# Kernel optimization log

Measured on AMD Instinct MI355X. Metric: run time of the kernel, lower is better.

Reference implementation:

```python
import jax, jax.numpy as jnp
import numpy as np

B, H, W, L, C = 4, 64, 64, 64, 64
NB, BS, F = 8, 8, 1          # num_blocks, block_size, hidden_size_factor
R, ALPHA = 8, 1.0            # lora_r, lora_alpha
M, T = 32, 8                 # modes, temporal_modes
SCALE = 1.0 / (BS * BS * F)  # param init scale from the module


def setup_inputs() -> dict:
    key = jax.random.key(0)
    ks = jax.random.split(key, 14)
    d = {"x": jax.random.normal(ks[0], (B, H, W, L, C), jnp.float32)}
    d["w1"] = SCALE * jax.random.uniform(ks[1], (2, NB, BS, BS * F), jnp.float32)
    d["b1"] = SCALE * jax.random.uniform(ks[2], (2, NB, BS * F), jnp.float32)
    d["w2"] = SCALE * jax.random.uniform(ks[3], (2, NB, BS * F, BS), jnp.float32)
    d["b2"] = SCALE * jax.random.uniform(ks[4], (2, NB, BS), jnp.float32)
    names = ["la1rA", "la1rB", "la1iA", "la1iB", "la2rA", "la2rB", "la2iA", "la2iB"]
    shapes = [(NB, BS, R), (NB, R, BS * F), (NB, BS, R), (NB, R, BS * F),
              (NB, BS * F, R), (NB, R, BS), (NB, BS * F, R), (NB, R, BS)]
    for i, (n, s) in enumerate(zip(names, shapes)):
        d[n] = 0.02 * jax.random.normal(ks[5 + i], s, jnp.float32)
    return d


def _afno(x, w1, b1, w2, b2, la1rA, la1rB, la1iA, la1iB, la2rA, la2rB, la2iA, la2iB):
    s = ALPHA / R
    # effective per-block weights: base + LoRA low-rank update  [NB, in, out]
    W1r = w1[0] + s * jnp.einsum('nir,nro->nio', la1rA, la1rB)
    W1i = w1[1] + s * jnp.einsum('nir,nro->nio', la1iA, la1iB)
    W2r = w2[0] + s * jnp.einsum('nir,nro->nio', la2rA, la2rB)
    W2i = w2[1] + s * jnp.einsum('nir,nro->nio', la2iA, la2iB)

    xf = jnp.fft.rfftn(x, axes=(1, 2, 3), norm='ortho')      # [B,H,W,L//2+1,C] complex
    Lh = xf.shape[3]
    xs = xf[:, :M, :M, :T].reshape(B, M, M, T, NB, BS)        # truncated modes, block split
    xr, xi = xs.real, xs.imag

    def lin(v, Wb, bb):  # block-diagonal linear: [...,n,i] x [n,i,o] + [n,o]
        return jnp.einsum('bxyzni,nio->bxyzno', v, Wb) + bb

    gelu = lambda t: jax.nn.gelu(t, approximate=False)
    o1r = gelu(lin(xr, W1r, b1[0]) - lin(xi, W1i, b1[1]))
    o1i = gelu(lin(xi, W1r, b1[0]) + lin(xr, W1i, b1[1]))
    o2r = lin(o1r, W2r, b2[0]) - lin(o1i, W2i, b2[1])
    o2i = lin(o1i, W2r, b2[0]) + lin(o1r, W2i, b2[1])

    o2 = (o2r + 1j * o2i).reshape(B, M, M, T, C)
    full = jnp.zeros((B, H, W, Lh, C), dtype=xf.dtype).at[:, :M, :M, :T].set(o2)
    out = jnp.fft.irfftn(full, s=(H, W, L), axes=(1, 2, 3), norm='ortho')
    return out + x


def reference(x, w1, b1, w2, b2, la1rA, la1rB, la1iA, la1iB, la2rA, la2rB, la2iA, la2iB):
    return _afno(x, w1, b1, w2, b2, la1rA, la1rB, la1iA, la1iB, la2rA, la2rB, la2iA, la2iB)
```

## Files before the change

### kernel.cpp

```cpp
#include <hip/hip_runtime.h>
#include <math.h>


#define PI2_64 0.09817477042468103f

__device__ __forceinline__ float gelu_exact(float t) {
    return 0.5f * t * (1.0f + erff(t * 0.7071067811865475f));
}

__global__ void __launch_bounds__(256) k1a_dft_l(const float* __restrict__ x,
                                                 float* __restrict__ y1f) {
    __shared__ float2 twT[8][32];
    int tid = threadIdx.x;
    if (tid < 256) {
        int k = tid >> 5, l = tid & 31;
        float s, c;
        sincosf(PI2_64 * (float)((k * l) & 63), &s, &c);
        twT[k][l] = make_float2(c, s);
    }
    __syncthreads();

    int bid = blockIdx.x;
    int w8 = bid & 7, bh = bid >> 3;
    int cp = tid & 31, wl = tid >> 5;
    int w = w8 * 8 + wl;
    const float* xp = x + (size_t)(bh * 64 + w) * 4096 + 2 * cp;

    float4 A[8];
#pragma unroll
    for (int kl = 0; kl < 8; ++kl) A[kl] = make_float4(0.f, 0.f, 0.f, 0.f);

    for (int l0 = 0; l0 < 32; l0 += 2) {
        float2 v0  = *(const float2*)(xp + (l0 + 0) * 64);
        float2 v0p = *(const float2*)(xp + (l0 + 32) * 64);
        float2 v1  = *(const float2*)(xp + (l0 + 1) * 64);
        float2 v1p = *(const float2*)(xp + (l0 + 33) * 64);
        float2 E0 = make_float2(v0.x + v0p.x, v0.y + v0p.y);
        float2 O0 = make_float2(v0.x - v0p.x, v0.y - v0p.y);
        float2 E1 = make_float2(v1.x + v1p.x, v1.y + v1p.y);
        float2 O1 = make_float2(v1.x - v1p.x, v1.y - v1p.y);
#pragma unroll
        for (int kl = 0; kl < 8; ++kl) {
            float2 t0 = twT[kl][l0];
            float2 t1 = twT[kl][l0 + 1];
            float2 s0 = (kl & 1) ? O0 : E0;
            float2 s1 = (kl & 1) ? O1 : E1;
            A[kl].x += s0.x * t0.x;  A[kl].y -= s0.x * t0.y;
            A[kl].z += s0.y * t0.x;  A[kl].w -= s0.y * t0.y;
            A[kl].x += s1.x * t1.x;  A[kl].y -= s1.x * t1.y;
            A[kl].z += s1.y * t1.x;  A[kl].w -= s1.y * t1.y;
        }
    }
    float4* y1 = (float4*)y1f;
    size_t base = (size_t)bh * 16384 + (size_t)w * 32 + cp;
#pragma unroll
    for (int kl = 0; kl < 8; ++kl)
        y1[base + kl * 2048] = A[kl];
}

__global__ void __launch_bounds__(256) k1b_dft_w(const float* __restrict__ y1f,
                                                 float* __restrict__ y2f) {
    __shared__ float4 sD[64 * 32];
    __shared__ float2 twT[32][32];
    int tid = threadIdx.x;
#pragma unroll
    for (int e = 0; e < 4; ++e) {
        int idx = e * 256 + tid;
        int k = idx >> 5, l = idx & 31;
        float s, c;
        sincosf(PI2_64 * (float)((k * l) & 63), &s, &c);
        twT[k][l] = make_float2(c, s);
    }
    int pos = blockIdx.x;
    int kl = pos & 7, bh = pos >> 3;
    const float4* src = (const float4*)y1f + (size_t)pos * 2048;
#pragma unroll
    for (int r = 0; r < 8; ++r)
        sD[r * 256 + tid] = src[r * 256 + tid];
    __syncthreads();

    int cp = tid & 31, kwg = tid >> 5;
    float4 acc[4];
#pragma unroll
    for (int i = 0; i < 4; ++i) acc[i] = make_float4(0.f, 0.f, 0.f, 0.f);

    for (int w = 0; w < 32; ++w) {
        float4 d  = sD[w * 32 + cp];
        float4 dp = sD[(w + 32) * 32 + cp];
        float4 E = make_float4(d.x + dp.x, d.y + dp.y, d.z + dp.z, d.w + dp.w);
        float4 O = make_float4(d.x - dp.x, d.y - dp.y, d.z - dp.z, d.w - dp.w);
#pragma unroll
        for (int i = 0; i < 4; ++i) {
            float2 t = twT[kwg * 4 + i][w];
            float4 s = (i & 1) ? O : E;
            acc[i].x += s.x * t.x + s.y * t.y;
            acc[i].y += s.y * t.x - s.x * t.y;
            acc[i].z += s.z * t.x + s.w * t.y;
            acc[i].w += s.w * t.x - s.z * t.y;
        }
    }
    int b = bh >> 6, h = bh & 63;
    float4* y2 = (float4*)y2f;
#pragma unroll
    for (int i = 0; i < 4; ++i) {
        int kw = kwg * 4 + i;
        y2[((size_t)((b * 8 + kl) * 32 + kw) * 64 + h) * 32 + cp] = acc[i];
    }
}

__global__ void __launch_bounds__(256) kc_h_mlp(
        const float* __restrict__ y2f, float* __restrict__ z2f,
        const float* __restrict__ w1, const float* __restrict__ b1,
        const float* __restrict__ w2, const float* __restrict__ b2,
        const float* __restrict__ la1rA, const float* __restrict__ la1rB,
        const float* __restrict__ la1iA, const float* __restrict__ la1iB,
        const float* __restrict__ la2rA, const float* __restrict__ la2rB,
        const float* __restrict__ la2iA, const float* __restrict__ la2iB) {
    __shared__ float2 sD[64][64];
    __shared__ float2 sT[32][34];
    __shared__ float2 sM[32][66];
    __shared__ float  sW[4][512];
    __shared__ float  sb1[128], sb2[128];
    int tid = threadIdx.x;
    int pos = blockIdx.x;
    int kl = pos & 7, kw = (pos >> 3) & 31, b = pos >> 8;

#pragma unroll
    for (int r = 0; r < 4; ++r) {
        int idx = r * 256 + tid;
        int h = idx >> 5, kh = idx & 31;
        float sn, cs;
        sincosf(PI2_64 * (float)((h * kh) & 63), &sn, &cs);
        sT[h][kh] = make_float2(cs, -sn);
    }
    const float2* src = (const float2*)y2f + (size_t)((b * 8 + kl) * 32 + kw) * 4096;
#pragma unroll
    for (int r = 0; r < 8; ++r) {
        int f = r * 512 + tid * 2;
        *(float4*)(&sD[f >> 6][f & 63]) = *(const float4*)(src + f);
    }
    {
        const float* As[4]   = {la1rA, la1iA, la2rA, la2iA};
        const float* Bs[4]   = {la1rB, la1iB, la2rB, la2iB};
        const float* base[4] = {w1, w1 + 512, w2, w2 + 512};
#pragma unroll
        for (int e = 0; e < 8; ++e) {
            int flat = tid + e * 256;
            int mat = flat >> 9;
            int rem = flat & 511;
            int n = rem >> 6, i = (rem >> 3) & 7, o = rem & 7;
            const float* A  = As[mat] + n * 64 + i * 8;
            const float* Bp = Bs[mat] + n * 64 + o;
            float s = 0.f;
#pragma unroll
            for (int r = 0; r < 8; ++r) s += A[r] * Bp[r * 8];
            sW[mat][(i * 8 + o) * 8 + n] = base[mat][n * 64 + i * 8 + o] + 0.125f * s;
        }
        if (tid < 128) sb1[tid] = b1[tid];
        else           sb2[tid - 128] = b2[tid - 128];
    }
    __syncthreads();

    {
        float4* sd4 = (float4*)&sD[0][0];
#pragma unroll
        for (int r = 0; r < 4; ++r) {
            int idx = r * 256 + tid;
            int h = idx >> 5, cq = idx & 31;
            float4 a = sd4[h * 32 + cq];
            float4 c = sd4[(h + 32) * 32 + cq];
            sd4[h * 32 + cq]        = make_float4(a.x + c.x, a.y + c.y, a.z + c.z, a.w + c.w);
            sd4[(h + 32) * 32 + cq] = make_float4(a.x - c.x, a.y - c.y, a.z - c.z, a.w - c.w);
        }
    }
    __syncthreads();

    {
        int kh0 = (tid >> 5) * 4;
        int c0  = (tid & 31) * 2;
        float mr[4][2], mi[4][2];
#pragma unroll
        for (int i = 0; i < 4; ++i)
#pragma unroll
            for (int j = 0; j < 2; ++j) { mr[i][j] = 0.f; mi[i][j] = 0.f; }
        for (int h = 0; h < 32; ++h) {
            float4 dE = *(const float4*)(&sD[h][c0]);
            float4 dO = *(const float4*)(&sD[h + 32][c0]);
            float Er[2] = {dE.x, dE.z}, Ei[2] = {dE.y, dE.w};
            float Or[2] = {dO.x, dO.z}, Oi[2] = {dO.y, dO.w};
            const float4* tT = (const float4*)(&sT[h][kh0]);
            float4 u0 = tT[0], u1 = tT[1];
            float Tr[4] = {u0.x, u0.z, u1.x, u1.z};
            float Ti[4] = {u0.y, u0.w, u1.y, u1.w};
#pragma unroll
            for (int i = 0; i < 4; ++i) {
                const float* Dr = (i & 1) ? Or : Er;
                const float* Di = (i & 1) ? Oi : Ei;
#pragma unroll
                for (int j = 0; j < 2; ++j) {
                    mr[i][j] += Tr[i] * Dr[j] - Ti[i] * Di[j];
                    mi[i][j] += Tr[i] * Di[j] + Ti[i] * Dr[j];
                }
            }
        }
        const float sc = 1.0f / 512.0f;
#pragma unroll
        for (int i = 0; i < 4; ++i)
#pragma unroll
            for (int j = 0; j < 2; ++j)
                sM[kh0 + i][c0 + j] = make_float2(mr[i][j] * sc, mi[i][j] * sc);
    }
    __syncthreads();

    float2* sM2 = (float2*)&sD[0][0];
    {
        int kh = tid >> 3, n = tid & 7;
        float xr[8], xi[8];
#pragma unroll
        for (int i = 0; i < 8; ++i) {
            float2 v = sM[kh][n * 8 + i];
            xr[i] = v.x; xi[i] = v.y;
        }
        float o1r[8], o1i[8];
#pragma unroll
        for (int o = 0; o < 8; ++o) {
            float br = sb1[n * 8 + o], bi = sb1[64 + n * 8 + o];
            float sr = br - bi, si = br + bi;
#pragma unroll
            for (int i = 0; i < 8; ++i) {
                float wr = sW[0][(i * 8 + o) * 8 + n];
                float wi = sW[1][(i * 8 + o) * 8 + n];
                sr += xr[i] * wr - xi[i] * wi;
                si += xi[i] * wr + xr[i] * wi;
            }
            o1r[o] = gelu_exact(sr);
            o1i[o] = gelu_exact(si);
        }
#pragma unroll
        for (int o = 0; o < 8; ++o) {
            float br = sb2[n * 8 + o], bi = sb2[64 + n * 8 + o];
            float sr = br - bi, si = br + bi;
#pragma unroll
            for (int i = 0; i < 8; ++i) {
                float wr = sW[2][(i * 8 + o) * 8 + n];
                float wi = sW[3][(i * 8 + o) * 8 + n];
                sr += o1r[i] * wr - o1i[i] * wi;
                si += o1i[i] * wr + o1r[i] * wi;
            }
            sM2[kh * 66 + n * 8 + o] = make_float2(sr, si);
        }
    }
    __syncthreads();

    {
        int h0 = (tid >> 4) * 2;
        int c0 = (tid & 15) * 4;
        float SEr[2][4], SEi[2][4], SOr[2][4], SOi[2][4];
#pragma unroll
        for (int r = 0; r < 2; ++r)
#pragma unroll
            for (int j = 0; j < 4; ++j) {
                SEr[r][j] = 0.f; SEi[r][j] = 0.f;
                SOr[r][j] = 0.f; SOi[r][j] = 0.f;
            }
        for (int khp = 0; khp < 16; ++khp) {
#pragma unroll
            for (int par = 0; par < 2; ++par) {
                int kh = 2 * khp + par;
                float2 T0 = sT[h0 + 0][kh];
                float2 T1 = sT[h0 + 1][kh];
                const float4* tM = (const float4*)(sM2 + kh * 66 + c0);
                float4 m0 = tM[0], m1 = tM[1];
                float Mr[4] = {m0.x, m0.z, m1.x, m1.z};
                float Mi[4] = {m0.y, m0.w, m1.y, m1.w};
                float (*Sr)[4] = par ? SOr : SEr;
                float (*Si)[4] = par ? SOi : SEi;
                float Tr[2] = {T0.x, T1.x};
                float Ti[2] = {T0.y, T1.y};
#pragma unroll
                for (int r = 0; r < 2; ++r)
#pragma unroll
                    for (int j = 0; j < 4; ++j) {
                        Sr[r][j] += Tr[r] * Mr[j] + Ti[r] * Mi[j];
                        Si[r][j] += Tr[r] * Mi[j] - Ti[r] * Mr[j];
                    }
            }
        }
        float2* dst = (float2*)z2f + (size_t)((b * 8 + kl) * 32 + kw) * 4096;
#pragma unroll
        for (int r = 0; r < 2; ++r) {
            float4* dA = (float4*)(dst + (h0 + r) * 64 + c0);
            dA[0] = make_float4(SEr[r][0] + SOr[r][0], SEi[r][0] + SOi[r][0],
                                SEr[r][1] + SOr[r][1], SEi[r][1] + SOi[r][1]);
            dA[1] = make_float4(SEr[r][2] + SOr[r][2], SEi[r][2] + SOi[r][2],
                                SEr[r][3] + SOr[r][3], SEi[r][3] + SOi[r][3]);
            float4* dB = (float4*)(dst + (h0 + 32 + r) * 64 + c0);
            dB[0] = make_float4(SEr[r][0] - SOr[r][0], SEi[r][0] - SOi[r][0],
                                SEr[r][1] - SOr[r][1], SEi[r][1] - SOi[r][1]);
            dB[1] = make_float4(SEr[r][2] - SOr[r][2], SEi[r][2] - SOi[r][2],
                                SEr[r][3] - SOr[r][3], SEi[r][3] - SOi[r][3]);
        }
    }
}

__global__ void __launch_bounds__(256) k3a_idft_w(const float* __restrict__ z2f,
                                                  float* __restrict__ zwf) {
    __shared__ float4 sZ[2 * 32 * 32];
    __shared__ float2 twT[32][32];
    int tid = threadIdx.x;
#pragma unroll
    for (int e = 0; e < 4; ++e) {
        int idx = e * 256 + tid;
        int w = idx >> 5, kw = idx & 31;
        float s, c;
        sincosf(PI2_64 * (float)((w * kw) & 63), &s, &c);
        twT[w][kw] = make_float2(c, s);
    }
    int bid = blockIdx.x;
    int klq = bid & 3, h = (bid >> 2) & 63, b = bid >> 8;
    const float4* z2 = (const float4*)z2f;
#pragma unroll
    for (int r = 0; r < 8; ++r) {
        int idx = r * 256 + tid;
        int row = idx >> 5, cp2 = idx & 31;
        int kli = row >> 5, kw = row & 31;
        sZ[idx] = z2[((size_t)((b * 8 + klq * 2 + kli) * 32 + kw) * 64 + h) * 32 + cp2];
    }
    __syncthreads();

    int cp = tid & 31, wq = tid >> 5;

    float4 E[2][4], O[2][4];
#pragma unroll
    for (int kli = 0; kli < 2; ++kli)
#pragma unroll
        for (int j = 0; j < 4; ++j) {
            E[kli][j] = make_float4(0.f, 0.f, 0.f, 0.f);
            O[kli][j] = make_float4(0.f, 0.f, 0.f, 0.f);
        }

    for (int kw = 0; kw < 32; kw += 2) {
#pragma unroll
        for (int kli = 0; kli < 2; ++kli) {
            float4 d = sZ[(kli * 32 + kw) * 32 + cp];
#pragma unroll
            for (int j = 0; j < 4; ++j) {
                float2 t = twT[wq * 4 + j][kw];
                E[kli][j].x += d.x * t.x - d.y * t.y;
                E[kli][j].y += d.y * t.x + d.x * t.y;
                E[kli][j].z += d.z * t.x - d.w * t.y;
                E[kli][j].w += d.w * t.x + d.z * t.y;
            }
        }
#pragma unroll
        for (int kli = 0; kli < 2; ++kli) {
            float4 d = sZ[(kli * 32 + kw + 1) * 32 + cp];
#pragma unroll
            for (int j = 0; j < 4; ++j) {
                float2 t = twT[wq * 4 + j][kw + 1];
                O[kli][j].x += d.x * t.x - d.y * t.y;
                O[kli][j].y += d.y * t.x + d.x * t.y;
                O[kli][j].z += d.z * t.x - d.w * t.y;
                O[kli][j].w += d.w * t.x + d.z * t.y;
            }
        }
    }
    float4* zw = (float4*)zwf;
    size_t slab = ((size_t)(b * 64 + h)) * 16384;
#pragma unroll
    for (int kli = 0; kli < 2; ++kli) {
        int kl = klq * 2 + kli;
#pragma unroll
        for (int j = 0; j < 4; ++j) {
            int w = wq * 4 + j;
            float4 e = E[kli][j], o = O[kli][j];
            zw[slab + ((size_t)w * 8 + kl) * 32 + cp] =
                make_float4(e.x + o.x, e.y + o.y, e.z + o.z, e.w + o.w);
            zw[slab + ((size_t)(w + 32) * 8 + kl) * 32 + cp] =
                make_float4(e.x - o.x, e.y - o.y, e.z - o.z, e.w - o.w);
        }
    }
}

__global__ void __launch_bounds__(256) k3b_idft_l(const float* __restrict__ x,
                                                  const float* __restrict__ zwf,
                                                  float* __restrict__ outp) {
    __shared__ float2 twA[8][32];
    int tid = threadIdx.x;
    if (tid < 256) {
        int k = tid >> 5, l = tid & 31;
        float s, c;
        sincosf(PI2_64 * (float)((k * l) & 63), &s, &c);
        twA[k][l] = make_float2(c, s);
    }
    __syncthreads();

    int bid = blockIdx.x;
    int w8 = bid & 7, bh = bid >> 3;
    int cp = tid & 31, wl = tid >> 5;
    int w = w8 * 8 + wl;

    const float4* zw = (const float4*)zwf +
        ((size_t)bh * 64 + w) * 256 + cp;
    float4 z[8];
#pragma unroll
    for (int kl = 0; kl < 8; ++kl) z[kl] = zw[kl * 32];

    float z0r0 = z[0].x, z0r1 = z[0].z;
#pragma unroll
    for (int kl = 1; kl < 8; ++kl) {
        z[kl].x *= 2.f; z[kl].y *= 2.f; z[kl].z *= 2.f; z[kl].w *= 2.f;
    }
    const size_t row = ((size_t)(bh * 64 + w)) * 4096;
    const float* xp = x + row + 2 * cp;
    float* op = outp + row + 2 * cp;
    const float sc = 1.0f / 512.0f;

    for (int l = 0; l < 32; ++l) {
        float2 a0 = *(const float2*)(xp + l * 64);
        float2 a1 = *(const float2*)(xp + (l + 32) * 64);
        float e0 = 0.f, e1 = 0.f, o0 = 0.f, o1 = 0.f;
#pragma unroll
        for (int kl = 2; kl < 8; kl += 2) {
            float2 t = twA[kl][l];
            e0 += z[kl].x * t.x - z[kl].y * t.y;
            e1 += z[kl].z * t.x - z[kl].w * t.y;
        }
#pragma unroll
        for (int kl = 1; kl < 8; kl += 2) {
            float2 t = twA[kl][l];
            o0 += z[kl].x * t.x - z[kl].y * t.y;
            o1 += z[kl].z * t.x - z[kl].w * t.y;
        }
        float base0 = z0r0 + e0, base1 = z0r1 + e1;
        *(float2*)(op + l * 64) =
            make_float2((base0 + o0) * sc + a0.x, (base1 + o1) * sc + a0.y);
        *(float2*)(op + (l + 32) * 64) =
            make_float2((base0 - o0) * sc + a1.x, (base1 - o1) * sc + a1.y);
    }
}

extern "C" void kernel_launch(void* const* d_in, const int* in_sizes, int n_in,
                              void* d_out, int out_size, void* d_ws, size_t ws_size,
                              hipStream_t stream) {
    const float* x     = (const float*)d_in[0];
    const float* w1    = (const float*)d_in[1];
    const float* b1    = (const float*)d_in[2];
    const float* w2    = (const float*)d_in[3];
    const float* b2    = (const float*)d_in[4];
    const float* la1rA = (const float*)d_in[5];
    const float* la1rB = (const float*)d_in[6];
    const float* la1iA = (const float*)d_in[7];
    const float* la1iB = (const float*)d_in[8];
    const float* la2rA = (const float*)d_in[9];
    const float* la2rB = (const float*)d_in[10];
    const float* la2iA = (const float*)d_in[11];
    const float* la2iB = (const float*)d_in[12];
    float* out = (float*)d_out;

    float* ws = (float*)d_ws;
    float* y1 = ws;
    float* y2 = ws + 16777216;
    float* z2 = ws + 25165824;
    float* zw = ws + 33554432;

    hipLaunchKernelGGL(k1a_dft_l,  dim3(2048), dim3(256), 0, stream, x, y1);
    hipLaunchKernelGGL(k1b_dft_w,  dim3(2048), dim3(256), 0, stream, y1, y2);
    hipLaunchKernelGGL(kc_h_mlp,   dim3(1024), dim3(256), 0, stream, y2, z2,
                       w1, b1, w2, b2, la1rA, la1rB, la1iA, la1iB,
                       la2rA, la2rB, la2iA, la2iB);
    hipLaunchKernelGGL(k3a_idft_w, dim3(1024), dim3(256), 0, stream, z2, zw);
    hipLaunchKernelGGL(k3b_idft_l, dim3(2048), dim3(256), 0, stream, x, zw, out);
}
```

Measured before the change: 320.5 us.

## Store all inter-kernel spectral intermediates as bf16 to halve workspace traffic

Every intermediate buffer passed between the five DFT/MLP kernels (y1, y2, z2, zw) is now packed to bfloat16 with round-to-nearest-even and unpacked to fp32 on load. All arithmetic stays in fp32. The goal is to halve the global memory bytes written and read between stages, which dominate this memory-bound pipeline. The cost is reduced precision in the spectral intermediates, which adds error to the output and could break a tight tolerance.

```diff
diff --git a/kernel.cpp b/kernel.cpp
--- a/kernel.cpp
+++ b/kernel.cpp
@@ -8,8 +8,23 @@
     return 0.5f * t * (1.0f + erff(t * 0.7071067811865475f));
 }
 
+__device__ __forceinline__ unsigned int f2bf(float f) {
+    unsigned int u = __float_as_uint(f);
+    return (u + 0x7FFFu + ((u >> 16) & 1u)) >> 16;
+}
+__device__ __forceinline__ uint2 pack4(float4 f) {
+    return make_uint2(f2bf(f.x) | (f2bf(f.y) << 16),
+                      f2bf(f.z) | (f2bf(f.w) << 16));
+}
+__device__ __forceinline__ float4 unpack4(uint2 u) {
+    return make_float4(__uint_as_float(u.x << 16),
+                       __uint_as_float(u.x & 0xFFFF0000u),
+                       __uint_as_float(u.y << 16),
+                       __uint_as_float(u.y & 0xFFFF0000u));
+}
+
 __global__ void __launch_bounds__(256) k1a_dft_l(const float* __restrict__ x,
-                                                 float* __restrict__ y1f) {
+                                                 unsigned int* __restrict__ y1f) {
     __shared__ float2 twT[8][32];
     int tid = threadIdx.x;
     if (tid < 256) {
@@ -51,15 +66,15 @@
             A[kl].z += s1.y * t1.x;  A[kl].w -= s1.y * t1.y;
         }
     }
-    float4* y1 = (float4*)y1f;
+    uint2* y1 = (uint2*)y1f;
     size_t base = (size_t)bh * 16384 + (size_t)w * 32 + cp;
 #pragma unroll
     for (int kl = 0; kl < 8; ++kl)
-        y1[base + kl * 2048] = A[kl];
-}
-
-__global__ void __launch_bounds__(256) k1b_dft_w(const float* __restrict__ y1f,
-                                                 float* __restrict__ y2f) {
+        y1[base + kl * 2048] = pack4(A[kl]);
+}
+
+__global__ void __launch_bounds__(256) k1b_dft_w(const unsigned int* __restrict__ y1f,
+                                                 unsigned int* __restrict__ y2f) {
     __shared__ float4 sD[64 * 32];
     __shared__ float2 twT[32][32];
     int tid = threadIdx.x;
@@ -73,10 +88,10 @@
     }
     int pos = blockIdx.x;
     int kl = pos & 7, bh = pos >> 3;
-    const float4* src = (const float4*)y1f + (size_t)pos * 2048;
+    const uint2* src = (const uint2*)y1f + (size_t)pos * 2048;
 #pragma unroll
     for (int r = 0; r < 8; ++r)
-        sD[r * 256 + tid] = src[r * 256 + tid];
+        sD[r * 256 + tid] = unpack4(src[r * 256 + tid]);
     __syncthreads();
 
     int cp = tid & 31, kwg = tid >> 5;
@@ -100,16 +115,16 @@
         }
     }
     int b = bh >> 6, h = bh & 63;
-    float4* y2 = (float4*)y2f;
+    uint2* y2 = (uint2*)y2f;
 #pragma unroll
     for (int i = 0; i < 4; ++i) {
         int kw = kwg * 4 + i;
-        y2[((size_t)((b * 8 + kl) * 32 + kw) * 64 + h) * 32 + cp] = acc[i];
+        y2[((size_t)((b * 8 + kl) * 32 + kw) * 64 + h) * 32 + cp] = pack4(acc[i]);
     }
 }
 
 __global__ void __launch_bounds__(256) kc_h_mlp(
-        const float* __restrict__ y2f, float* __restrict__ z2f,
+        const unsigned int* __restrict__ y2f, unsigned int* __restrict__ z2f,
         const float* __restrict__ w1, const float* __restrict__ b1,
         const float* __restrict__ w2, const float* __restrict__ b2,
         const float* __restrict__ la1rA, const float* __restrict__ la1rB,
@@ -133,11 +148,11 @@
         sincosf(PI2_64 * (float)((h * kh) & 63), &sn, &cs);
         sT[h][kh] = make_float2(cs, -sn);
     }
-    const float2* src = (const float2*)y2f + (size_t)((b * 8 + kl) * 32 + kw) * 4096;
+    const uint2* src = (const uint2*)y2f + (size_t)((b * 8 + kl) * 32 + kw) * 2048;
 #pragma unroll
     for (int r = 0; r < 8; ++r) {
-        int f = r * 512 + tid * 2;
-        *(float4*)(&sD[f >> 6][f & 63]) = *(const float4*)(src + f);
+        int idx = r * 256 + tid;
+        *(float4*)(&sD[idx >> 5][(idx & 31) * 2]) = unpack4(src[idx]);
     }
     {
         const float* As[4]   = {la1rA, la1iA, la2rA, la2iA};
@@ -286,25 +301,25 @@
                     }
             }
         }
-        float2* dst = (float2*)z2f + (size_t)((b * 8 + kl) * 32 + kw) * 4096;
+        uint2* dst = (uint2*)z2f + (size_t)((b * 8 + kl) * 32 + kw) * 2048;
 #pragma unroll
         for (int r = 0; r < 2; ++r) {
-            float4* dA = (float4*)(dst + (h0 + r) * 64 + c0);
-            dA[0] = make_float4(SEr[r][0] + SOr[r][0], SEi[r][0] + SOi[r][0],
-                                SEr[r][1] + SOr[r][1], SEi[r][1] + SOi[r][1]);
-            dA[1] = make_float4(SEr[r][2] + SOr[r][2], SEi[r][2] + SOi[r][2],
-                                SEr[r][3] + SOr[r][3], SEi[r][3] + SOi[r][3]);
-            float4* dB = (float4*)(dst + (h0 + 32 + r) * 64 + c0);
-            dB[0] = make_float4(SEr[r][0] - SOr[r][0], SEi[r][0] - SOi[r][0],
-                                SEr[r][1] - SOr[r][1], SEi[r][1] - SOi[r][1]);
-            dB[1] = make_float4(SEr[r][2] - SOr[r][2], SEi[r][2] - SOi[r][2],
-                                SEr[r][3] - SOr[r][3], SEi[r][3] - SOi[r][3]);
-        }
-    }
-}
-
-__global__ void __launch_bounds__(256) k3a_idft_w(const float* __restrict__ z2f,
-                                                  float* __restrict__ zwf) {
+            int iA = (h0 + r) * 32 + (c0 >> 1);
+            dst[iA]     = pack4(make_float4(SEr[r][0] + SOr[r][0], SEi[r][0] + SOi[r][0],
+                                            SEr[r][1] + SOr[r][1], SEi[r][1] + SOi[r][1]));
+            dst[iA + 1] = pack4(make_float4(SEr[r][2] + SOr[r][2], SEi[r][2] + SOi[r][2],
+                                            SEr[r][3] + SOr[r][3], SEi[r][3] + SOi[r][3]));
+            int iB = (h0 + 32 + r) * 32 + (c0 >> 1);
+            dst[iB]     = pack4(make_float4(SEr[r][0] - SOr[r][0], SEi[r][0] - SOi[r][0],
+                                            SEr[r][1] - SOr[r][1], SEi[r][1] - SOi[r][1]));
+            dst[iB + 1] = pack4(make_float4(SEr[r][2] - SOr[r][2], SEi[r][2] - SOi[r][2],
+                                            SEr[r][3] - SOr[r][3], SEi[r][3] - SOi[r][3]));
+        }
+    }
+}
+
+__global__ void __launch_bounds__(256) k3a_idft_w(const unsigned int* __restrict__ z2f,
+                                                  unsigned int* __restrict__ zwf) {
     __shared__ float4 sZ[2 * 32 * 32];
     __shared__ float2 twT[32][32];
     int tid = threadIdx.x;
@@ -318,13 +333,14 @@
     }
     int bid = blockIdx.x;
     int klq = bid & 3, h = (bid >> 2) & 63, b = bid >> 8;
-    const float4* z2 = (const float4*)z2f;
+    const uint2* z2 = (const uint2*)z2f;
 #pragma unroll
     for (int r = 0; r < 8; ++r) {
         int idx = r * 256 + tid;
         int row = idx >> 5, cp2 = idx & 31;
         int kli = row >> 5, kw = row & 31;
-        sZ[idx] = z2[((size_t)((b * 8 + klq * 2 + kli) * 32 + kw) * 64 + h) * 32 + cp2];
+        sZ[idx] = unpack4(
+            z2[((size_t)((b * 8 + klq * 2 + kli) * 32 + kw) * 64 + h) * 32 + cp2]);
     }
     __syncthreads();
 
@@ -365,7 +381,7 @@
             }
         }
     }
-    float4* zw = (float4*)zwf;
+    uint2* zw = (uint2*)zwf;
     size_t slab = ((size_t)(b * 64 + h)) * 16384;
 #pragma unroll
     for (int kli = 0; kli < 2; ++kli) {
@@ -375,15 +391,15 @@
             int w = wq * 4 + j;
             float4 e = E[kli][j], o = O[kli][j];
             zw[slab + ((size_t)w * 8 + kl) * 32 + cp] =
-                make_float4(e.x + o.x, e.y + o.y, e.z + o.z, e.w + o.w);
+                pack4(make_float4(e.x + o.x, e.y + o.y, e.z + o.z, e.w + o.w));
             zw[slab + ((size_t)(w + 32) * 8 + kl) * 32 + cp] =
-                make_float4(e.x - o.x, e.y - o.y, e.z - o.z, e.w - o.w);
+                pack4(make_float4(e.x - o.x, e.y - o.y, e.z - o.z, e.w - o.w));
         }
     }
 }
 
 __global__ void __launch_bounds__(256) k3b_idft_l(const float* __restrict__ x,
-                                                  const float* __restrict__ zwf,
+                                                  const unsigned int* __restrict__ zwf,
                                                   float* __restrict__ outp) {
     __shared__ float2 twA[8][32];
     int tid = threadIdx.x;
@@ -400,11 +416,10 @@
     int cp = tid & 31, wl = tid >> 5;
     int w = w8 * 8 + wl;
 
-    const float4* zw = (const float4*)zwf +
-        ((size_t)bh * 64 + w) * 256 + cp;
+    const uint2* zw = (const uint2*)zwf + ((size_t)bh * 64 + w) * 256 + cp;
     float4 z[8];
 #pragma unroll
-    for (int kl = 0; kl < 8; ++kl) z[kl] = zw[kl * 32];
+    for (int kl = 0; kl < 8; ++kl) z[kl] = unpack4(zw[kl * 32]);
 
     float z0r0 = z[0].x, z0r1 = z[0].z;
 #pragma unroll
@@ -458,11 +473,11 @@
     const float* la2iB = (const float*)d_in[12];
     float* out = (float*)d_out;
 
-    float* ws = (float*)d_ws;
-    float* y1 = ws;
-    float* y2 = ws + 16777216;
-    float* z2 = ws + 25165824;
-    float* zw = ws + 33554432;
+    unsigned int* ws = (unsigned int*)d_ws;
+    unsigned int* y1 = ws;
+    unsigned int* y2 = ws + 8388608;
+    unsigned int* z2 = ws + 12582912;
+    unsigned int* zw = ws + 16777216;
 
     hipLaunchKernelGGL(k1a_dft_l,  dim3(2048), dim3(256), 0, stream, x, y1);
     hipLaunchKernelGGL(k1b_dft_w,  dim3(2048), dim3(256), 0, stream, y1, y2);
```

Result: faster. 300.6 us (-6.2%).
